# Kernel tuning notes

Measured on AMD Instinct MI355X. Metric: run time of the kernel, lower is better.

Reference implementation:

```python
import jax, jax.numpy as jnp
import numpy as np

EPS = 1e-6


def smooth(p):
    # smooth_distribution: clamp Bernoulli params away from {0,1}
    return jnp.clip(p, EPS, 1.0 - EPS)


def bern_logprob(p, x):
    # Bernoulli(p).log_prob(x) = x*log(p) + (1-x)*log(1-p)
    return x * jnp.log(p) + (1.0 - x) * jnp.log1p(-p)


def binary_row_reduce(A, b, k):
    # GF(2) Gaussian elimination on [A | b]; A:(k,n) binary float, b:(k,)
    M = jnp.concatenate([A, b[:, None]], axis=1)  # (k, n+1)
    rows = jnp.arange(k)
    for i in range(k):  # k is a small static int (25)
        col = M[:, i]
        cand = jnp.where((rows >= i) & (col > 0.5), rows, k)
        p = jnp.minimum(jnp.min(cand), k - 1)  # pivot row (fallback k-1 if none; prob ~0 for random A)
        ri, rp = M[i], M[p]
        M = M.at[i].set(rp)
        M = M.at[p].set(ri)
        elim = (M[:, i] > 0.5) & (rows != i)
        M = jnp.where(elim[:, None], jnp.mod(M + M[i], 2.0), M)
    return M[:, :-1], M[:, -1]


def compute_term1(logq, logp):
    # stable [sum_s q*log p]/[sum_s q], summed over batch; logq,logp: (S,B)
    m = jnp.max(logq, axis=0)                                  # (B,)
    w = jnp.exp(logq - m)                                      # (S,B)
    neg_num = m + jnp.log(jnp.sum(w * (-logp), axis=0))
    pos_den = m + jnp.log(jnp.sum(w, axis=0))
    return -jnp.sum(jnp.exp(neg_num - pos_den))


def setup_inputs() -> dict:
    key = jax.random.key(0)
    ks = jax.random.split(key, 5)
    nx, nz, B = 2048, 256, 512
    wr = float(np.sqrt(6.0 / (nx + nz)))
    xr = float(np.sqrt(6.0 / nx))
    zr = float(np.sqrt(6.0 / nz))
    U = jax.random.uniform(ks[0], (nz, nx), minval=-wr, maxval=wr)
    V = jax.random.uniform(ks[1], (nx, nz), minval=-wr, maxval=wr)
    x_bias = jax.random.uniform(ks[2], (nx,), minval=-xr, maxval=xr)
    z_bias = jax.random.uniform(ks[3], (nz,), minval=-zr, maxval=zr)
    xin = (jax.random.uniform(ks[4], (B, nx)) < 0.5).astype(jnp.float32)
    return {"xin": xin, "U": U, "V": V, "x_bias": x_bias, "z_bias": z_bias,
            "S": 10, "k": 25, "T": 30}


def reference(xin, U, V, x_bias, z_bias, S, k, T):
    dt = xin.dtype
    key = jax.random.key(42)
    kz, kx, kA, kb = jax.random.split(key, 4)

    # q(z|x) and samples  -------------------------------------------------
    q = smooth(jax.nn.sigmoid(xin @ U.T + z_bias))                     # (B, nz)
    samples_z = (jax.random.uniform(kz, (S,) + q.shape) < q).astype(dt)  # (S,B,nz)
    ps = smooth(jax.nn.sigmoid(jnp.einsum('sbz,xz->sbx', samples_z, V) + x_bias))  # (S,B,nx)
    xouts = (jax.random.uniform(kx, ps.shape) < ps).astype(dt)

    # projected ELBO over T random GF(2) hash constraints ------------------
    nz = U.shape[0]
    A_all = (jax.random.uniform(kA, (T, k, nz)) < 0.5).astype(dt)
    b_all = (jax.random.uniform(kb, (T, k)) < 0.5).astype(dt)
    pz = smooth(jax.nn.sigmoid(z_bias))                                # (nz,)

    def elbo_t(carry, Ab):
        A, b = Ab
        C, bp = binary_row_reduce(A, b, k)                             # (k,nz),(k,)
        proj = jnp.mod(jnp.einsum('sbz,kz->sbk', samples_z[:, :, k:], C[:, k:]) + bp, 2.0)
        sz = samples_z.at[:, :, :k].set(proj)                          # (S,B,nz)
        logq_zi = bern_logprob(q, sz).sum(axis=2)                      # (S,B)
        logp_z = bern_logprob(pz, sz).sum(axis=2)                      # (S,B)
        ps_t = smooth(jax.nn.sigmoid(jnp.einsum('sbz,xz->sbx', sz, V) + x_bias))
        logp_x = bern_logprob(ps_t, xin).sum(axis=2)                   # (S,B)
        logp = logp_z + logp_x
        term2 = compute_term1(logq_zi, logq_zi)
        term1 = compute_term1(logq_zi, logp)
        return carry, term1 - term2

    _, pelbos = jax.lax.scan(elbo_t, 0.0, (A_all, b_all))
    loss = -jnp.mean(pelbos)
    return q, samples_z, ps, xouts, loss
```

## Files before the change

### kernel.cpp

```cpp
#include <hip/hip_runtime.h>
#include <cstdint>

#define NX 2048
#define NZ 256
#define NB 512
#define NS 10
#define NK 25
#define NT 30
#define SBTOT (NS * NB)

#define LOG2E 1.4426950408889634f
#define LN2 0.6931471805599453f

#define OFF_Q 0
#define OFF_SAMP (NB * NZ)
#define OFF_PS (OFF_SAMP + SBTOT * NZ)
#define OFF_XO (OFF_PS + SBTOT * NX)
#define OFF_LOSS (OFF_XO + SBTOT * NX)

typedef unsigned long long ull;
typedef __bf16 bf16x8 __attribute__((ext_vector_type(8)));
typedef float f32x4 __attribute__((ext_vector_type(4)));
typedef uint32_t u32x2 __attribute__((ext_vector_type(2)));

__host__ __device__ inline void tf2x32(uint32_t k0, uint32_t k1, uint32_t x0, uint32_t x1,
                                       uint32_t& o0, uint32_t& o1) {
  uint32_t k2 = k0 ^ k1 ^ 0x1BD11BDAu;
  x0 += k0; x1 += k1;
#define TF_R(r) { x0 += x1; x1 = (x1 << (r)) | (x1 >> (32 - (r))); x1 ^= x0; }
  TF_R(13) TF_R(15) TF_R(26) TF_R(6)
  x0 += k1; x1 += k2 + 1u;
  TF_R(17) TF_R(29) TF_R(16) TF_R(24)
  x0 += k2; x1 += k0 + 2u;
  TF_R(13) TF_R(15) TF_R(26) TF_R(6)
  x0 += k0; x1 += k1 + 3u;
  TF_R(17) TF_R(29) TF_R(16) TF_R(24)
  x0 += k1; x1 += k2 + 4u;
  TF_R(13) TF_R(15) TF_R(26) TF_R(6)
  x0 += k2; x1 += k0 + 5u;
#undef TF_R
  o0 = x0; o1 = x1;
}

__device__ inline uint32_t tf_select(uint32_t k0, uint32_t k1, uint32_t i, uint32_t h) {
  bool lo = i < h;
  uint32_t x0 = lo ? i : i - h;
  uint32_t x1 = lo ? i + h : i;
  uint32_t o0, o1;
  tf2x32(k0, k1, x0, x1, o0, o1);
  return lo ? o0 : o1;
}

__device__ inline float tf_uniform(uint32_t k0, uint32_t k1, uint32_t i, uint32_t h) {
  uint32_t r = tf_select(k0, k1, i, h);
  return __uint_as_float(0x3f800000u | (r >> 9)) - 1.0f;
}

__device__ inline float sigclip(float a) {
  float p = 1.0f / (1.0f + __expf(-a));
  return fminf(fmaxf(p, 1e-6f), 1.0f - 1e-6f);
}

__device__ inline ushort f2bf(float f) {
  uint32_t u = __float_as_uint(f);
  return (ushort)((u + 0x7FFFu + ((u >> 16) & 1u)) >> 16);
}

__device__ inline float blockReduceSum256(float v, volatile float* s4) {
#pragma unroll
  for (int o = 32; o > 0; o >>= 1) v += __shfl_down(v, o);
  __syncthreads();
  if ((threadIdx.x & 63) == 0) s4[threadIdx.x >> 6] = v;
  __syncthreads();
  return s4[0] + s4[1] + s4[2] + s4[3];
}

__global__ __launch_bounds__(256) void kP0_prep(const float* __restrict__ V,
                                                const float* __restrict__ U,
                                                const float* __restrict__ xin,
                                                const float* __restrict__ z_bias,
                                                ushort* __restrict__ Vbf,
                                                ushort* __restrict__ Vkpad2,
                                                ushort* __restrict__ Uhi,
                                                ushort* __restrict__ Ulo,
                                                ushort* __restrict__ xinbf,
                                                float* __restrict__ baseq,
                                                float* __restrict__ d_lpz,
                                                float* __restrict__ basepz,
                                                double* __restrict__ loss_acc,
                                                uint32_t* __restrict__ done_ctr) {
  __shared__ float red[4];
  int tid = threadIdx.x;
  int e = blockIdx.x * 256 + tid;
  {
    int x = e >> 8, k = e & 255;
    float v = V[e];
    Vbf[e] = f2bf(v);
    if (k < 32) Vkpad2[x * 32 + k] = (k < NK) ? f2bf(v * LOG2E) : (ushort)0;
  }
  {
    float u = U[e];
    ushort hi = f2bf(u);
    Uhi[e] = hi;
    float hv = __uint_as_float((uint32_t)hi << 16);
    Ulo[e] = f2bf(u - hv);
  }
  {
    xinbf[e] = (xin[e] > 0.5f) ? (ushort)0x3F80 : (ushort)0;
    int e2 = e + NX * NZ;
    xinbf[e2] = (xin[e2] > 0.5f) ? (ushort)0x3F80 : (ushort)0;
  }
  if (e < NB) baseq[e] = 0.0f;
  if (blockIdx.x == 0) {
    if (tid == 0) { *loss_acc = 0.0; *done_ctr = 0u; }
    int z = tid;
    float pz = sigclip(z_bias[z]);
    float lp = __logf(pz), l1 = __logf(1.0f - pz);
    d_lpz[z] = lp - l1;
    float s = blockReduceSum256(l1, red);
    if (z == 0) *basepz = s;
  }
}

__global__ __launch_bounds__(256) void k1w_mfma(const ushort* __restrict__ xinbf,
                                                const ushort* __restrict__ Uhi,
                                                const ushort* __restrict__ Ulo,
                                                const float* __restrict__ z_bias,
                                                const float* __restrict__ xin,
                                                const ushort* __restrict__ Vkpad2,
                                                float* __restrict__ outq,
                                                float* __restrict__ d_lq,
                                                float* __restrict__ baseq,
                                                float* __restrict__ W,
                                                ull* __restrict__ Ct,
                                                uint32_t* __restrict__ bpmask,
                                                uint32_t kA0, uint32_t kA1,
                                                uint32_t kb0, uint32_t kb1) {
  __shared__ float red[4][16][17];
  __shared__ float wred[4][NK];
  __shared__ uint32_t Aw[NK][8];
  __shared__ uint32_t bbsh[NK];
  int tid = threadIdx.x;
  if (blockIdx.x >= 1024) {
    int t = blockIdx.x - 1024;
    if (tid < NK * 8) {
      int r = tid >> 3, c = tid & 7;
      const uint32_t hA = (uint32_t)NT * NK * NZ / 2;
      uint32_t base_i = (uint32_t)(t * NK + r) * NZ + c * 32;
      uint32_t w = 0;
      for (int zz = 0; zz < 32; ++zz) {
        uint32_t rr = tf_select(kA0, kA1, base_i + zz, hA);
        w |= ((rr >> 31) ^ 1u) << zz;
      }
      Aw[r][c] = w;
    }
    if (tid < NK) {
      const uint32_t hb = (uint32_t)NT * NK / 2;
      uint32_t rb = tf_select(kb0, kb1, (uint32_t)(t * NK + tid), hb);
      bbsh[tid] = (rb >> 31) ^ 1u;
    }
    __syncthreads();
    if (tid >= 64) return;
    int lane = tid;
    ull w0 = 0, w1 = 0, w2 = 0, w3 = 0;
    uint32_t bbit = 0;
    if (lane < NK) {
      w0 = (ull)Aw[lane][0] | ((ull)Aw[lane][1] << 32);
      w1 = (ull)Aw[lane][2] | ((ull)Aw[lane][3] << 32);
      w2 = (ull)Aw[lane][4] | ((ull)Aw[lane][5] << 32);
      w3 = (ull)Aw[lane][6] | ((ull)Aw[lane][7] << 32);
      bbit = bbsh[lane];
    }
    for (int i = 0; i < NK; ++i) {
      int mybit = (int)((w0 >> i) & 1ull);
      ull mask = __ballot(lane < NK && mybit);
      ull cand = mask & (~0ull << i);
      int p = cand ? __builtin_ctzll(cand) : (NK - 1);
      int srcl = (lane == i) ? p : ((lane == p) ? i : lane);
      w0 = __shfl(w0, srcl); w1 = __shfl(w1, srcl); w2 = __shfl(w2, srcl); w3 = __shfl(w3, srcl);
      bbit = __shfl(bbit, srcl);
      ull p0 = __shfl(w0, i), p1 = __shfl(w1, i), p2 = __shfl(w2, i), p3 = __shfl(w3, i);
      uint32_t pvb = __shfl(bbit, i);
      int nb2 = (int)((w0 >> i) & 1ull);
      if (lane < NK && lane != i && nb2) {
        w0 ^= p0; w1 ^= p1; w2 ^= p2; w3 ^= p3; bbit ^= pvb;
      }
    }
    if (lane < NK) {
      w0 &= ~((1ull << NK) - 1ull);
      ull* dstp = Ct + (size_t)(t * NK + lane) * 4;
      dstp[0] = w0; dstp[1] = w1; dstp[2] = w2; dstp[3] = w3;
    }
    ull bm = __ballot(lane < NK && bbit);
    if (lane == 0) bpmask[t] = (uint32_t)bm & 0x1FFFFFFu;
    return;
  }
  if (blockIdx.x < 512) {
    int wave = tid >> 6, lane = tid & 63, grp = lane >> 4, col = lane & 15;
    int b0 = (blockIdx.x >> 4) * 16;
    int z0 = (blockIdx.x & 15) * 16;
    f32x4 acc = {0.f, 0.f, 0.f, 0.f};
    const ushort* arow = xinbf + (size_t)(b0 + col) * NX + wave * 512 + grp * 8;
    const ushort* bhr = Uhi + (size_t)(z0 + col) * NX + wave * 512 + grp * 8;
    const ushort* blr = Ulo + (size_t)(z0 + col) * NX + wave * 512 + grp * 8;
#pragma unroll 4
    for (int s = 0; s < 16; ++s) {
      bf16x8 a = *(const bf16x8*)(arow + s * 32);
      bf16x8 bh = *(const bf16x8*)(bhr + s * 32);
      bf16x8 bl = *(const bf16x8*)(blr + s * 32);
      acc = __builtin_amdgcn_mfma_f32_16x16x32_bf16(a, bh, acc, 0, 0, 0);
      acc = __builtin_amdgcn_mfma_f32_16x16x32_bf16(a, bl, acc, 0, 0, 0);
    }
#pragma unroll
    for (int r = 0; r < 4; ++r) red[wave][grp * 4 + r][col] = acc[r];
    __syncthreads();
    int bi = tid >> 4, zi = tid & 15;
    float aa = red[0][bi][zi] + red[1][bi][zi] + red[2][bi][zi] + red[3][bi][zi] + z_bias[z0 + zi];
    int b = b0 + bi, z = z0 + zi;
    float q = sigclip(aa);
    outq[b * NZ + z] = q;
    float lq = __logf(q), l1 = __logf(1.0f - q);
    d_lq[b * NZ + z] = lq - l1;
    float s1 = l1;
#pragma unroll
    for (int o = 1; o < 16; o <<= 1) s1 += __shfl_xor(s1, o);
    if (zi == 0) atomicAdd(&baseq[b], s1);
    return;
  }
  int b = blockIdx.x - 512;
  float acc[NK];
#pragma unroll
  for (int j = 0; j < NK; ++j) acc[j] = 0.0f;
#pragma unroll
  for (int i = 0; i < 8; ++i) {
    int x = i * 256 + tid;
    float s = 1.0f - 2.0f * xin[(size_t)b * NX + x];
    const uint4* vp = (const uint4*)(Vkpad2 + (size_t)x * 32);
    uint4 q0 = vp[0], q1 = vp[1], q2 = vp[2], q3 = vp[3];
    uint32_t w[16] = {q0.x, q0.y, q0.z, q0.w, q1.x, q1.y, q1.z, q1.w,
                      q2.x, q2.y, q2.z, q2.w, q3.x, q3.y, q3.z, q3.w};
#pragma unroll
    for (int j = 0; j < NK; ++j) {
      uint32_t wd = w[j >> 1];
      float v = __uint_as_float((j & 1) ? (wd & 0xFFFF0000u) : (wd << 16));
      acc[j] = fmaf(s, v, acc[j]);
    }
  }
#pragma unroll
  for (int j = 0; j < NK; ++j) {
#pragma unroll
    for (int o = 1; o < 64; o <<= 1) acc[j] += __shfl_xor(acc[j], o);
  }
  if ((tid & 63) == 0) {
#pragma unroll
    for (int j = 0; j < NK; ++j) wred[tid >> 6][j] = acc[j];
  }
  __syncthreads();
  if (tid < NK) W[b * 32 + tid] = wred[0][tid] + wred[1][tid] + wred[2][tid] + wred[3][tid];
}

__global__ __launch_bounds__(256) void k2_samples(const float* __restrict__ q,
                                                  const float* __restrict__ d_lq,
                                                  const float* __restrict__ d_lpz,
                                                  const ull* __restrict__ Ct,
                                                  const uint32_t* __restrict__ bpmask,
                                                  const float* __restrict__ W,
                                                  float* __restrict__ samp_out,
                                                  ushort* __restrict__ samp16,
                                                  ull* __restrict__ Spack,
                                                  float* __restrict__ qtail,
                                                  float* __restrict__ ptail,
                                                  uint32_t* __restrict__ projb,
                                                  float* __restrict__ Syd,
                                                  uint32_t kz0, uint32_t kz1) {
  __shared__ float red[4];
  __shared__ ull sp_sh[4];
  int sb = blockIdx.x;
  int z = threadIdx.x;
  int b = sb & (NB - 1);
  uint32_t i = (uint32_t)sb * NZ + z;
  const uint32_t h = (uint32_t)SBTOT * NZ / 2;
  float u = tf_uniform(kz0, kz1, i, h);
  float qv = q[b * NZ + z];
  int smp = (u < qv) ? 1 : 0;
  __builtin_nontemporal_store((float)smp, samp_out + i);
  samp16[i] = smp ? (ushort)0x3F80 : (ushort)0;
  ull m = __ballot(smp);
  if ((z & 63) == 0) { Spack[sb * 4 + (z >> 6)] = m; sp_sh[z >> 6] = m; }
  float dq = (z >= NK && smp) ? d_lq[b * NZ + z] : 0.0f;
  float dp = (z >= NK && smp) ? d_lpz[z] : 0.0f;
  float sq = blockReduceSum256(dq, red);
  float sp = blockReduceSum256(dp, red);
  if (z == 0) { qtail[sb] = sq; ptail[sb] = sp; }
  if (z < 32) {
    int t = z;
    ull s0 = sp_sh[0], s1 = sp_sh[1], s2 = sp_sh[2], s3 = sp_sh[3];
    uint32_t s25 = (uint32_t)(s0 & 0x1FFFFFFull);
    const float* Wb = W + (size_t)b * 32;
    uint32_t out;
    float syd = 0.0f;
    if (t < NT) {
      uint32_t bp = bpmask[t];
      uint32_t pb = 0;
#pragma unroll
      for (int j = 0; j < NK; ++j) {
        const ull* C = Ct + (size_t)(t * NK + j) * 4;
        int par = __popcll(s0 & C[0]) + __popcll(s1 & C[1]) + __popcll(s2 & C[2]) + __popcll(s3 & C[3]);
        uint32_t bit = ((uint32_t)(par ^ (int)(bp >> j))) & 1u;
        pb |= bit << j;
        int d = (int)bit - (int)((s25 >> j) & 1u);
        syd = fmaf((float)d, Wb[j], syd);
      }
      out = pb;
    } else {
      out = s25;
    }
    projb[sb * 32 + t] = out;
    Syd[sb * 32 + t] = syd;
  }
}

__global__ __launch_bounds__(256) void k3m_gemm(const ushort* __restrict__ samp16,
                                                const ushort* __restrict__ Vbf,
                                                const float* __restrict__ x_bias,
                                                ushort* __restrict__ base2,
                                                float* __restrict__ ps_out,
                                                float* __restrict__ xo_out,
                                                uint32_t kx0, uint32_t kx1) {
  __shared__ __align__(16) char smem[2 * 2112 * 4];
  ushort* As = (ushort*)smem;
  ushort* Bs = (ushort*)(smem + 8192);
  float* Tt = (float*)smem;

  int tid = threadIdx.x;
  int wave = tid >> 6, lane = tid & 63, grp = lane >> 4, col = lane & 15;
  int x0 = blockIdx.x * 128;
  int sb0 = blockIdx.y * 32;
  f32x4 acc[2][4];
#pragma unroll
  for (int mi = 0; mi < 2; ++mi)
#pragma unroll
    for (int ni = 0; ni < 4; ++ni) acc[mi][ni] = (f32x4){0.f, 0.f, 0.f, 0.f};

  for (int k0 = 0; k0 < NZ; k0 += 32) {
    {
      int rowb = tid >> 2, kcb = (tid & 3) << 3;
      int sbrow = (rowb < 32) ? (sb0 + rowb) : (sb0 + 2528 + rowb);
      *(uint4*)&Bs[rowb * 32 + kcb] = *(const uint4*)&samp16[(size_t)sbrow * NZ + k0 + kcb];
#pragma unroll
      for (int c = tid; c < 512; c += 256) {
        int rowa = c >> 2, kca = (c & 3) << 3;
        *(uint4*)&As[rowa * 32 + kca] = *(const uint4*)&Vbf[(size_t)(x0 + rowa) * NZ + k0 + kca];
      }
    }
    __syncthreads();
    bf16x8 af[2], bfv[4];
#pragma unroll
    for (int mi = 0; mi < 2; ++mi)
      af[mi] = *(const bf16x8*)&As[(wave * 32 + mi * 16 + col) * 32 + grp * 8];
#pragma unroll
    for (int ni = 0; ni < 4; ++ni)
      bfv[ni] = *(const bf16x8*)&Bs[(ni * 16 + col) * 32 + grp * 8];
#pragma unroll
    for (int mi = 0; mi < 2; ++mi)
#pragma unroll
      for (int ni = 0; ni < 4; ++ni)
        acc[mi][ni] = __builtin_amdgcn_mfma_f32_16x16x32_bf16(af[mi], bfv[ni], acc[mi][ni], 0, 0, 0);
    __syncthreads();
  }

  const uint32_t HH = (uint32_t)(SBTOT / 2) * (uint32_t)NX;
#pragma unroll
  for (int pi = 0; pi < 2; ++pi) {
    __syncthreads();
#pragma unroll
    for (int mi = 0; mi < 2; ++mi) {
      int cbase = wave * 32 + mi * 16 + grp * 4;
      *(float4*)&Tt[col * 132 + cbase] = *(float4*)&acc[mi][pi];
      *(float4*)&Tt[2112 + col * 132 + cbase] = *(float4*)&acc[mi][pi + 2];
    }
    __syncthreads();
#pragma unroll
    for (int pass = 0; pass < 2; ++pass) {
      int r = pass * 8 + (tid >> 5);
      int c = (tid & 31) * 4;
      float4 t0 = *(float4*)&Tt[r * 132 + c];
      float4 t1 = *(float4*)&Tt[2112 + r * 132 + c];
      float4 xb4 = *(const float4*)(x_bias + x0 + c);
      int sb_a = sb0 + pi * 16 + r;
      size_t off_a = (size_t)sb_a * NX + x0 + c;
      size_t off_b = off_a + (size_t)HH;
      float a0 = t0.x + xb4.x, a1 = t0.y + xb4.y, a2 = t0.z + xb4.z, a3 = t0.w + xb4.w;
      float b0 = t1.x + xb4.x, b1 = t1.y + xb4.y, b2 = t1.z + xb4.z, b3 = t1.w + xb4.w;
      u32x2 bpa, bpb;
      bpa[0] = (uint32_t)f2bf(a0 * LOG2E) | ((uint32_t)f2bf(a1 * LOG2E) << 16);
      bpa[1] = (uint32_t)f2bf(a2 * LOG2E) | ((uint32_t)f2bf(a3 * LOG2E) << 16);
      bpb[0] = (uint32_t)f2bf(b0 * LOG2E) | ((uint32_t)f2bf(b1 * LOG2E) << 16);
      bpb[1] = (uint32_t)f2bf(b2 * LOG2E) | ((uint32_t)f2bf(b3 * LOG2E) << 16);
      *(u32x2*)(base2 + off_a) = bpa;
      *(u32x2*)(base2 + off_b) = bpb;
      f32x4 pva = {sigclip(a0), sigclip(a1), sigclip(a2), sigclip(a3)};
      f32x4 pvb = {sigclip(b0), sigclip(b1), sigclip(b2), sigclip(b3)};
      __builtin_nontemporal_store(pva, (f32x4*)(ps_out + off_a));
      __builtin_nontemporal_store(pvb, (f32x4*)(ps_out + off_b));
      uint32_t fi = (uint32_t)off_a;
      uint32_t r0, r1;
      f32x4 xva, xvb;
      tf2x32(kx0, kx1, fi + 0u, fi + 0u + HH, r0, r1);
      xva[0] = ((__uint_as_float(0x3f800000u | (r0 >> 9)) - 1.0f) < pva[0]) ? 1.0f : 0.0f;
      xvb[0] = ((__uint_as_float(0x3f800000u | (r1 >> 9)) - 1.0f) < pvb[0]) ? 1.0f : 0.0f;
      tf2x32(kx0, kx1, fi + 1u, fi + 1u + HH, r0, r1);
      xva[1] = ((__uint_as_float(0x3f800000u | (r0 >> 9)) - 1.0f) < pva[1]) ? 1.0f : 0.0f;
      xvb[1] = ((__uint_as_float(0x3f800000u | (r1 >> 9)) - 1.0f) < pvb[1]) ? 1.0f : 0.0f;
      tf2x32(kx0, kx1, fi + 2u, fi + 2u + HH, r0, r1);
      xva[2] = ((__uint_as_float(0x3f800000u | (r0 >> 9)) - 1.0f) < pva[2]) ? 1.0f : 0.0f;
      xvb[2] = ((__uint_as_float(0x3f800000u | (r1 >> 9)) - 1.0f) < pvb[2]) ? 1.0f : 0.0f;
      tf2x32(kx0, kx1, fi + 3u, fi + 3u + HH, r0, r1);
      xva[3] = ((__uint_as_float(0x3f800000u | (r0 >> 9)) - 1.0f) < pva[3]) ? 1.0f : 0.0f;
      xvb[3] = ((__uint_as_float(0x3f800000u | (r1 >> 9)) - 1.0f) < pvb[3]) ? 1.0f : 0.0f;
      __builtin_nontemporal_store(xva, (f32x4*)(xo_out + off_a));
      __builtin_nontemporal_store(xvb, (f32x4*)(xo_out + off_b));
    }
  }
}

__global__ __launch_bounds__(256) void k6_mfma(const ushort* __restrict__ base2,
                                               const ushort* __restrict__ Vkpad2,
                                               const float* __restrict__ xin,
                                               const uint32_t* __restrict__ projb,
                                               const ull* __restrict__ Spack,
                                               const float* __restrict__ Syd,
                                               float* __restrict__ logpx) {
  __shared__ float bvsm[NX];
  __shared__ float lsum[4][32];
  __shared__ float red[4];
  int sb = blockIdx.x;
  int b = sb & (NB - 1);
  int tid = threadIdx.x;
  int wave = tid >> 6, lane = tid & 63;
  int grp = lane >> 4, col = lane & 15;
  const uint4* b16p = (const uint4*)(base2 + (size_t)sb * NX);
  const float4* x4p = (const float4*)(xin + (size_t)b * NX);
  float sbacc = 0.0f;
  {
    uint4 bu = b16p[tid];
    float4 xv0 = x4p[tid * 2], xv1 = x4p[tid * 2 + 1];
    uint32_t wds[4] = {bu.x, bu.y, bu.z, bu.w};
    float bv[8];
#pragma unroll
    for (int j = 0; j < 8; ++j) {
      uint32_t wd = wds[j >> 1];
      bv[j] = __uint_as_float((j & 1) ? (wd & 0xFFFF0000u) : (wd << 16));
    }
    float sg[8] = {1.0f - 2.0f * xv0.x, 1.0f - 2.0f * xv0.y, 1.0f - 2.0f * xv0.z,
                   1.0f - 2.0f * xv0.w, 1.0f - 2.0f * xv1.x, 1.0f - 2.0f * xv1.y,
                   1.0f - 2.0f * xv1.z, 1.0f - 2.0f * xv1.w};
#pragma unroll
    for (int j = 0; j < 8; ++j) {
      bvsm[tid * 8 + j] = bv[j];
      sbacc = fmaf(sg[j], bv[j], sbacc);
    }
  }
  float Sb = blockReduceSum256(sbacc, red);
  uint32_t s25 = (uint32_t)(Spack[sb * 4] & 0x1FFFFFFull);
  uint32_t pb0 = projb[sb * 32 + col];
  uint32_t pb1 = projb[sb * 32 + 16 + col];
  bf16x8 a0, a1;
  union { ushort u; __bf16 hh; } cvt;
#pragma unroll
  for (int j = 0; j < 8; ++j) {
    int k = grp * 8 + j;
    int sbit = (int)((s25 >> k) & 1u);
    int d0 = (int)((pb0 >> k) & 1u) - sbit;
    int d1 = (int)((pb1 >> k) & 1u) - sbit;
    cvt.u = (ushort)(d0 == 0 ? 0 : (d0 > 0 ? 0x3F80 : 0xBF80)); a0[j] = cvt.hh;
    cvt.u = (ushort)(d1 == 0 ? 0 : (d1 > 0 ? 0x3F80 : 0xBF80)); a1[j] = cvt.hh;
  }
  float acca[8], pp[8];
#pragma unroll
  for (int r = 0; r < 8; ++r) { acca[r] = 0.0f; pp[r] = 1.0f; }
  const ushort* vkbase = Vkpad2 + (size_t)(wave * 512 + col) * 32 + grp * 8;
  const float* bvp = bvsm + wave * 512 + col;
#pragma unroll 4
  for (int i = 0; i < 32; ++i) {
    float bs = bvp[i * 16];
    bf16x8 bfr = *(const bf16x8*)(vkbase + (size_t)i * 16 * 32);
    f32x4 cb = {bs, bs, bs, bs};
    f32x4 c0 = __builtin_amdgcn_mfma_f32_16x16x32_bf16(a0, bfr, cb, 0, 0, 0);
    f32x4 c1 = __builtin_amdgcn_mfma_f32_16x16x32_bf16(a1, bfr, cb, 0, 0, 0);
#pragma unroll
    for (int r = 0; r < 4; ++r) {
      float y0 = c0[r];
      acca[r] += fabsf(y0);
      pp[r] = fmaf(pp[r], __builtin_amdgcn_exp2f(-fabsf(y0)), pp[r]);
      float y1 = c1[r];
      acca[4 + r] += fabsf(y1);
      pp[4 + r] = fmaf(pp[4 + r], __builtin_amdgcn_exp2f(-fabsf(y1)), pp[4 + r]);
    }
  }
#pragma unroll
  for (int r = 0; r < 8; ++r) {
    float m = 0.5f * acca[r] + __log2f(pp[r]);
#pragma unroll
    for (int off = 1; off < 16; off <<= 1) m += __shfl_xor(m, off);
    if (col == 0) {
      int t = (r < 4) ? (grp * 4 + r) : (16 + grp * 4 + (r - 4));
      lsum[wave][t] = m;
    }
  }
  __syncthreads();
  if (tid < NT) {
    float tot = lsum[0][tid] + lsum[1][tid] + lsum[2][tid] + lsum[3][tid];
    tot += 0.5f * (Sb + Syd[sb * 32 + tid]);
    logpx[(size_t)tid * SBTOT + sb] = -LN2 * tot;
  }
}

__global__ __launch_bounds__(64) void k7_reduce(const float* __restrict__ logpx,
                                                const uint32_t* __restrict__ projb,
                                                const float* __restrict__ qtail,
                                                const float* __restrict__ ptail,
                                                const float* __restrict__ baseq,
                                                const float* __restrict__ d_lq,
                                                const float* __restrict__ d_lpz,
                                                const float* __restrict__ basepz,
                                                double* __restrict__ loss_acc,
                                                uint32_t* __restrict__ done_ctr,
                                                float* __restrict__ out_loss) {
  int t = blockIdx.x;
  int chunk = blockIdx.y;
  int lane = threadIdx.x;
  int b = chunk * 64 + lane;
  float dlq[NK];
#pragma unroll
  for (int j = 0; j < NK; ++j) dlq[j] = d_lq[b * NZ + j];
  float bq = baseq[b];
  float bpz = *basepz;
  float lq[NS], lp[NS];
#pragma unroll
  for (int s = 0; s < NS; ++s) {
    int sb = s * NB + b;
    uint32_t m = projb[sb * 32 + t];
    float sq = 0.0f, spv = 0.0f;
#pragma unroll
    for (int j = 0; j < NK; ++j) {
      float on = (float)((m >> j) & 1u);
      sq += on * dlq[j];
      spv += on * d_lpz[j];
    }
    lq[s] = bq + qtail[sb] + sq;
    lp[s] = logpx[t * SBTOT + sb] + bpz + ptail[sb] + spv;
  }
  float mx = lq[0];
#pragma unroll
  for (int s = 1; s < NS; ++s) mx = fmaxf(mx, lq[s]);
  float den = 0.0f, num = 0.0f;
#pragma unroll
  for (int s = 0; s < NS; ++s) {
    float w = __expf(lq[s] - mx);
    den += w;
    num += w * (lq[s] - lp[s]);
  }
  double v = (double)(num / den);
#pragma unroll
  for (int o = 32; o > 0; o >>= 1) v += __shfl_down(v, o);
  if (lane == 0) {
    atomicAdd(loss_acc, v);
    __threadfence();
    uint32_t old = atomicAdd(done_ctr, 1u);
    if (old == (uint32_t)(NT * 8 - 1)) {
      double tot = atomicAdd(loss_acc, 0.0);
      *out_loss = (float)(tot / (double)NT);
    }
  }
}

extern "C" void kernel_launch(void* const* d_in, const int* in_sizes, int n_in,
                              void* d_out, int out_size, void* d_ws, size_t ws_size,
                              hipStream_t stream) {
  const float* xin = (const float*)d_in[0];
  const float* U = (const float*)d_in[1];
  const float* V = (const float*)d_in[2];
  const float* x_bias = (const float*)d_in[3];
  const float* z_bias = (const float*)d_in[4];
  float* out = (float*)d_out;

  char* p = (char*)d_ws;
  ushort* base2 = (ushort*)p;             p += (size_t)SBTOT * NX * 2;
  float* d_lq = (float*)p;                p += (size_t)NB * NZ * 4;
  float* baseq = (float*)p;               p += (size_t)NB * 4;
  float* d_lpz = (float*)p;               p += (size_t)NZ * 4;
  float* basepz = (float*)p;              p += 16;
  ull* Spack = (ull*)p;                   p += (size_t)SBTOT * 4 * 8;
  float* qtail = (float*)p;               p += (size_t)SBTOT * 4;
  float* ptail = (float*)p;               p += (size_t)SBTOT * 4;
  ull* Ct = (ull*)p;                      p += (size_t)NT * NK * 4 * 8;
  uint32_t* bpm = (uint32_t*)p;           p += 128;
  uint32_t* projb = (uint32_t*)p;         p += (size_t)SBTOT * 32 * 4;
  float* Syd = (float*)p;                 p += (size_t)SBTOT * 32 * 4;
  float* logpx = (float*)p;               p += (size_t)NT * SBTOT * 4;
  double* loss_acc = (double*)p;          p += 64;
  uint32_t* done_ctr = (uint32_t*)p;      p += 64;
  ushort* Vkpad2 = (ushort*)p;            p += (size_t)NX * 32 * 2;
  ushort* Vbf = (ushort*)p;               p += (size_t)NX * NZ * 2;
  ushort* samp16 = (ushort*)p;            p += (size_t)SBTOT * NZ * 2;
  float* W = (float*)p;                   p += (size_t)NB * 32 * 4;
  ushort* Uhi = (ushort*)p;               p += (size_t)NZ * NX * 2;
  ushort* Ulo = (ushort*)p;               p += (size_t)NZ * NX * 2;
  ushort* xinbf = (ushort*)p;             p += (size_t)NB * NX * 2;
  (void)ws_size; (void)in_sizes; (void)n_in; (void)out_size;

  uint32_t o0[4], o1[4];
  for (int j = 0; j < 4; ++j) tf2x32(0u, 42u, (uint32_t)j, (uint32_t)(4 + j), o0[j], o1[j]);
  uint32_t kz0 = o0[0], kz1 = o0[1];
  uint32_t kx0 = o0[2], kx1 = o0[3];
  uint32_t kA0 = o1[0], kA1 = o1[1];
  uint32_t kb0 = o1[2], kb1 = o1[3];

  kP0_prep<<<NX * NZ / 256, 256, 0, stream>>>(V, U, xin, z_bias, Vbf, Vkpad2,
                                              Uhi, Ulo, xinbf, baseq, d_lpz, basepz,
                                              loss_acc, done_ctr);
  k1w_mfma<<<1024 + NT, 256, 0, stream>>>(xinbf, Uhi, Ulo, z_bias, xin, Vkpad2,
                                          out + OFF_Q, d_lq, baseq, W,
                                          Ct, bpm, kA0, kA1, kb0, kb1);
  k2_samples<<<SBTOT, 256, 0, stream>>>(out + OFF_Q, d_lq, d_lpz, Ct, bpm, W,
                                        out + OFF_SAMP, samp16, Spack, qtail, ptail,
                                        projb, Syd, kz0, kz1);
  dim3 g3(NX / 128, SBTOT / 64);
  k3m_gemm<<<g3, 256, 0, stream>>>(samp16, Vbf, x_bias, base2,
                                   out + OFF_PS, out + OFF_XO, kx0, kx1);
  k6_mfma<<<SBTOT, 256, 0, stream>>>(base2, Vkpad2, xin, projb, Spack, Syd, logpx);
  dim3 g7(NT, 8);
  k7_reduce<<<g7, 64, 0, stream>>>(logpx, projb, qtail, ptail, baseq, d_lq,
                                   d_lpz, basepz, loss_acc, done_ctr, out + OFF_LOSS);
}
```

Measured before the change: 254.6 us.

## Split GEMM and logpx kernels into staged launches that overlap their work

The k3m GEMM is split into two parts: the first 40 row-tiles run on their own, and the remaining 40 row-tiles are co-scheduled in one mixed launch with k6 logpx blocks whose base2 inputs are already complete. A final k6 launch covers the remaining samples. The goal is to fill the GPU tail and overlap the compute-bound GEMM with the exp-heavy k6 work instead of serialising them. Separately, k6 now starts the MFMAs from zero and adds the bias afterwards instead of passing it as the accumulator, which may change register pressure. In exchange the change adds an extra launch and a divergent mixed kernel whose shared-memory size may limit k6 occupancy.

```diff
diff --git a/kernel.cpp b/kernel.cpp
--- a/kernel.cpp
+++ b/kernel.cpp
@@ -320,22 +320,20 @@
   }
 }
 
-__global__ __launch_bounds__(256) void k3m_gemm(const ushort* __restrict__ samp16,
-                                                const ushort* __restrict__ Vbf,
-                                                const float* __restrict__ x_bias,
-                                                ushort* __restrict__ base2,
-                                                float* __restrict__ ps_out,
-                                                float* __restrict__ xo_out,
-                                                uint32_t kx0, uint32_t kx1) {
-  __shared__ __align__(16) char smem[2 * 2112 * 4];
+__device__ inline void k3m_body(int x0, int sb0, char* smem,
+                                const ushort* __restrict__ samp16,
+                                const ushort* __restrict__ Vbf,
+                                const float* __restrict__ x_bias,
+                                ushort* __restrict__ base2,
+                                float* __restrict__ ps_out,
+                                float* __restrict__ xo_out,
+                                uint32_t kx0, uint32_t kx1) {
   ushort* As = (ushort*)smem;
   ushort* Bs = (ushort*)(smem + 8192);
   float* Tt = (float*)smem;
 
   int tid = threadIdx.x;
   int wave = tid >> 6, lane = tid & 63, grp = lane >> 4, col = lane & 15;
-  int x0 = blockIdx.x * 128;
-  int sb0 = blockIdx.y * 32;
   f32x4 acc[2][4];
 #pragma unroll
   for (int mi = 0; mi < 2; ++mi)
@@ -424,17 +422,17 @@
   }
 }
 
-__global__ __launch_bounds__(256) void k6_mfma(const ushort* __restrict__ base2,
-                                               const ushort* __restrict__ Vkpad2,
-                                               const float* __restrict__ xin,
-                                               const uint32_t* __restrict__ projb,
-                                               const ull* __restrict__ Spack,
-                                               const float* __restrict__ Syd,
-                                               float* __restrict__ logpx) {
-  __shared__ float bvsm[NX];
-  __shared__ float lsum[4][32];
-  __shared__ float red[4];
-  int sb = blockIdx.x;
+__device__ inline void k6_body(int sb, char* smem,
+                               const ushort* __restrict__ base2,
+                               const ushort* __restrict__ Vkpad2,
+                               const float* __restrict__ xin,
+                               const uint32_t* __restrict__ projb,
+                               const ull* __restrict__ Spack,
+                               const float* __restrict__ Syd,
+                               float* __restrict__ logpx) {
+  float* bvsm = (float*)smem;
+  float (*lsum)[32] = (float(*)[32])(smem + 8192);
+  float* red = (float*)(smem + 8704);
   int b = sb & (NB - 1);
   int tid = threadIdx.x;
   int wave = tid >> 6, lane = tid & 63;
@@ -480,20 +478,20 @@
 #pragma unroll
   for (int r = 0; r < 8; ++r) { acca[r] = 0.0f; pp[r] = 1.0f; }
   const ushort* vkbase = Vkpad2 + (size_t)(wave * 512 + col) * 32 + grp * 8;
-  const float* bvp = bvsm + wave * 512 + col;
 #pragma unroll 4
   for (int i = 0; i < 32; ++i) {
-    float bs = bvp[i * 16];
+    int x = (wave * 32 + i) * 16 + col;
     bf16x8 bfr = *(const bf16x8*)(vkbase + (size_t)i * 16 * 32);
-    f32x4 cb = {bs, bs, bs, bs};
-    f32x4 c0 = __builtin_amdgcn_mfma_f32_16x16x32_bf16(a0, bfr, cb, 0, 0, 0);
-    f32x4 c1 = __builtin_amdgcn_mfma_f32_16x16x32_bf16(a1, bfr, cb, 0, 0, 0);
+    f32x4 c0 = {0.f, 0.f, 0.f, 0.f}, c1 = {0.f, 0.f, 0.f, 0.f};
+    c0 = __builtin_amdgcn_mfma_f32_16x16x32_bf16(a0, bfr, c0, 0, 0, 0);
+    c1 = __builtin_amdgcn_mfma_f32_16x16x32_bf16(a1, bfr, c1, 0, 0, 0);
+    float bs = bvsm[x];
 #pragma unroll
     for (int r = 0; r < 4; ++r) {
-      float y0 = c0[r];
+      float y0 = bs + c0[r];
       acca[r] += fabsf(y0);
       pp[r] = fmaf(pp[r], __builtin_amdgcn_exp2f(-fabsf(y0)), pp[r]);
-      float y1 = c1[r];
+      float y1 = bs + c1[r];
       acca[4 + r] += fabsf(y1);
       pp[4 + r] = fmaf(pp[4 + r], __builtin_amdgcn_exp2f(-fabsf(y1)), pp[4 + r]);
     }
@@ -514,6 +512,57 @@
     tot += 0.5f * (Sb + Syd[sb * 32 + tid]);
     logpx[(size_t)tid * SBTOT + sb] = -LN2 * tot;
   }
+}
+
+__global__ __launch_bounds__(256) void k3m_gemm(const ushort* __restrict__ samp16,
+                                                const ushort* __restrict__ Vbf,
+                                                const float* __restrict__ x_bias,
+                                                ushort* __restrict__ base2,
+                                                float* __restrict__ ps_out,
+                                                float* __restrict__ xo_out,
+                                                uint32_t kx0, uint32_t kx1,
+                                                int ybase) {
+  __shared__ __align__(16) char smem[2 * 2112 * 4];
+  k3m_body(blockIdx.x * 128, (ybase + blockIdx.y) * 32, smem,
+           samp16, Vbf, x_bias, base2, ps_out, xo_out, kx0, kx1);
+}
+
+__global__ __launch_bounds__(256) void k36_mix(const ushort* __restrict__ samp16,
+                                               const ushort* __restrict__ Vbf,
+                                               const float* __restrict__ x_bias,
+                                               ushort* __restrict__ base2,
+                                               float* __restrict__ ps_out,
+                                               float* __restrict__ xo_out,
+                                               uint32_t kx0, uint32_t kx1,
+                                               const ushort* __restrict__ Vkpad2,
+                                               const float* __restrict__ xin,
+                                               const uint32_t* __restrict__ projb,
+                                               const ull* __restrict__ Spack,
+                                               const float* __restrict__ Syd,
+                                               float* __restrict__ logpx) {
+  __shared__ __align__(16) char smem[2 * 2112 * 4];
+  int bx = blockIdx.x;
+  if (bx < 640) {
+    k3m_body((bx & 15) * 128, (40 + (bx >> 4)) * 32, smem,
+             samp16, Vbf, x_bias, base2, ps_out, xo_out, kx0, kx1);
+  } else {
+    int i = bx - 640;
+    int sb = (i < 1280) ? i : i + 1280;
+    k6_body(sb, smem, base2, Vkpad2, xin, projb, Spack, Syd, logpx);
+  }
+}
+
+__global__ __launch_bounds__(256) void k6_solo(const ushort* __restrict__ base2,
+                                               const ushort* __restrict__ Vkpad2,
+                                               const float* __restrict__ xin,
+                                               const uint32_t* __restrict__ projb,
+                                               const ull* __restrict__ Spack,
+                                               const float* __restrict__ Syd,
+                                               float* __restrict__ logpx) {
+  __shared__ __align__(16) char smem[8720];
+  int i = blockIdx.x;
+  int sb = (i < 1280) ? (1280 + i) : (2560 + i);
+  k6_body(sb, smem, base2, Vkpad2, xin, projb, Spack, Syd, logpx);
 }
 
 __global__ __launch_bounds__(64) void k7_reduce(const float* __restrict__ logpx,
@@ -626,11 +675,15 @@
   k2_samples<<<SBTOT, 256, 0, stream>>>(out + OFF_Q, d_lq, d_lpz, Ct, bpm, W,
                                         out + OFF_SAMP, samp16, Spack, qtail, ptail,
                                         projb, Syd, kz0, kz1);
-  dim3 g3(NX / 128, SBTOT / 64);
-  k3m_gemm<<<g3, 256, 0, stream>>>(samp16, Vbf, x_bias, base2,
-                                   out + OFF_PS, out + OFF_XO, kx0, kx1);
-  k6_mfma<<<SBTOT, 256, 0, stream>>>(base2, Vkpad2, xin, projb, Spack, Syd, logpx);
+  dim3 g3a(NX / 128, 40);
+  k3m_gemm<<<g3a, 256, 0, stream>>>(samp16, Vbf, x_bias, base2,
+                                    out + OFF_PS, out + OFF_XO, kx0, kx1, 0);
+  k36_mix<<<640 + 2560, 256, 0, stream>>>(samp16, Vbf, x_bias, base2,
+                                          out + OFF_PS, out + OFF_XO, kx0, kx1,
+                                          Vkpad2, xin, projb, Spack, Syd, logpx);
+  k6_solo<<<2560, 256, 0, stream>>>(base2, Vkpad2, xin, projb, Spack, Syd, logpx);
   dim3 g7(NT, 8);
   k7_reduce<<<g7, 64, 0, stream>>>(logpx, projb, qtail, ptail, baseq, d_lq,
-                                   d_lpz, basepz, loss_acc, done_ctr, out + OFF_LOSS);
-}
+                                   d_lpz, basepz, loss_acc, done_ctr,
+                                   out + OFF_LOSS);
+}
```

Result: slower. 281.9 us (+10.7%).

## Fuse decoder GEMM with per-constraint logpx MFMA kernel via shared-memory tile

Applied to the files above, without the earlier changes.

Merges the decoder GEMM kernel and the per-constraint log p(x) kernel into one. The bf16 logits stay in shared memory for the block's 64 sample rows and 128 x-columns instead of going through a global base2 buffer. Each block computes partial logpx sums for its x-slice and accumulates them with atomicAdd into logpx, which k2 now zero-initialises. This removes the global write and re-read of the logits and one launch. In exchange it adds 16 atomics per row per constraint, doubles shared memory per block, and makes the float summation order nondeterministic.

```diff
diff --git a/kernel.cpp b/kernel.cpp
--- a/kernel.cpp
+++ b/kernel.cpp
@@ -272,6 +272,7 @@
                                                   float* __restrict__ ptail,
                                                   uint32_t* __restrict__ projb,
                                                   float* __restrict__ Syd,
+                                                  float* __restrict__ logpx,
                                                   uint32_t kz0, uint32_t kz1) {
   __shared__ float red[4];
   __shared__ ull sp_sh[4];
@@ -312,6 +313,7 @@
         syd = fmaf((float)d, Wb[j], syd);
       }
       out = pb;
+      logpx[(size_t)t * SBTOT + sb] = 0.0f;
     } else {
       out = s25;
     }
@@ -320,17 +322,23 @@
   }
 }
 
-__global__ __launch_bounds__(256) void k3m_gemm(const ushort* __restrict__ samp16,
-                                                const ushort* __restrict__ Vbf,
-                                                const float* __restrict__ x_bias,
-                                                ushort* __restrict__ base2,
-                                                float* __restrict__ ps_out,
-                                                float* __restrict__ xo_out,
-                                                uint32_t kx0, uint32_t kx1) {
-  __shared__ __align__(16) char smem[2 * 2112 * 4];
+__global__ __launch_bounds__(256) void k36_fused(const ushort* __restrict__ samp16,
+                                                 const ushort* __restrict__ Vbf,
+                                                 const float* __restrict__ x_bias,
+                                                 const ushort* __restrict__ Vkpad2,
+                                                 const float* __restrict__ xin,
+                                                 const uint32_t* __restrict__ projb,
+                                                 const ull* __restrict__ Spack,
+                                                 const float* __restrict__ Syd,
+                                                 float* __restrict__ ps_out,
+                                                 float* __restrict__ xo_out,
+                                                 float* __restrict__ logpx,
+                                                 uint32_t kx0, uint32_t kx1) {
+  __shared__ __align__(16) char smem[16896 + 16896];
   ushort* As = (ushort*)smem;
   ushort* Bs = (ushort*)(smem + 8192);
   float* Tt = (float*)smem;
+  ushort* bs16 = (ushort*)(smem + 16896);
 
   int tid = threadIdx.x;
   int wave = tid >> 6, lane = tid & 63, grp = lane >> 4, col = lane & 15;
@@ -387,7 +395,8 @@
       float4 t0 = *(float4*)&Tt[r * 132 + c];
       float4 t1 = *(float4*)&Tt[2112 + r * 132 + c];
       float4 xb4 = *(const float4*)(x_bias + x0 + c);
-      int sb_a = sb0 + pi * 16 + r;
+      int rowa = pi * 16 + r;
+      int sb_a = sb0 + rowa;
       size_t off_a = (size_t)sb_a * NX + x0 + c;
       size_t off_b = off_a + (size_t)HH;
       float a0 = t0.x + xb4.x, a1 = t0.y + xb4.y, a2 = t0.z + xb4.z, a3 = t0.w + xb4.w;
@@ -397,8 +406,8 @@
       bpa[1] = (uint32_t)f2bf(a2 * LOG2E) | ((uint32_t)f2bf(a3 * LOG2E) << 16);
       bpb[0] = (uint32_t)f2bf(b0 * LOG2E) | ((uint32_t)f2bf(b1 * LOG2E) << 16);
       bpb[1] = (uint32_t)f2bf(b2 * LOG2E) | ((uint32_t)f2bf(b3 * LOG2E) << 16);
-      *(u32x2*)(base2 + off_a) = bpa;
-      *(u32x2*)(base2 + off_b) = bpb;
+      *(u32x2*)&bs16[rowa * 132 + c] = bpa;
+      *(u32x2*)&bs16[(32 + rowa) * 132 + c] = bpb;
       f32x4 pva = {sigclip(a0), sigclip(a1), sigclip(a2), sigclip(a3)};
       f32x4 pvb = {sigclip(b0), sigclip(b1), sigclip(b2), sigclip(b3)};
       __builtin_nontemporal_store(pva, (f32x4*)(ps_out + off_a));
@@ -422,97 +431,68 @@
       __builtin_nontemporal_store(xvb, (f32x4*)(xo_out + off_b));
     }
   }
-}
-
-__global__ __launch_bounds__(256) void k6_mfma(const ushort* __restrict__ base2,
-                                               const ushort* __restrict__ Vkpad2,
-                                               const float* __restrict__ xin,
-                                               const uint32_t* __restrict__ projb,
-                                               const ull* __restrict__ Spack,
-                                               const float* __restrict__ Syd,
-                                               float* __restrict__ logpx) {
-  __shared__ float bvsm[NX];
-  __shared__ float lsum[4][32];
-  __shared__ float red[4];
-  int sb = blockIdx.x;
-  int b = sb & (NB - 1);
-  int tid = threadIdx.x;
-  int wave = tid >> 6, lane = tid & 63;
-  int grp = lane >> 4, col = lane & 15;
-  const uint4* b16p = (const uint4*)(base2 + (size_t)sb * NX);
-  const float4* x4p = (const float4*)(xin + (size_t)b * NX);
-  float sbacc = 0.0f;
-  {
-    uint4 bu = b16p[tid];
-    float4 xv0 = x4p[tid * 2], xv1 = x4p[tid * 2 + 1];
-    uint32_t wds[4] = {bu.x, bu.y, bu.z, bu.w};
-    float bv[8];
+  __syncthreads();
+
+  for (int s = 0; s < 16; ++s) {
+    int rowl = wave * 16 + s;
+    int sb = (rowl < 32) ? (sb0 + rowl) : (sb0 + 2528 + rowl);
+    int b = sb & (NB - 1);
+    uint32_t s25 = (uint32_t)(Spack[sb * 4] & 0x1FFFFFFull);
+    uint32_t pb0 = projb[sb * 32 + col];
+    uint32_t pb1 = projb[sb * 32 + 16 + col];
+    bf16x8 a0, a1;
+    union { ushort u; __bf16 hh; } cvt;
 #pragma unroll
     for (int j = 0; j < 8; ++j) {
-      uint32_t wd = wds[j >> 1];
-      bv[j] = __uint_as_float((j & 1) ? (wd & 0xFFFF0000u) : (wd << 16));
-    }
-    float sg[8] = {1.0f - 2.0f * xv0.x, 1.0f - 2.0f * xv0.y, 1.0f - 2.0f * xv0.z,
-                   1.0f - 2.0f * xv0.w, 1.0f - 2.0f * xv1.x, 1.0f - 2.0f * xv1.y,
-                   1.0f - 2.0f * xv1.z, 1.0f - 2.0f * xv1.w};
-#pragma unroll
-    for (int j = 0; j < 8; ++j) {
-      bvsm[tid * 8 + j] = bv[j];
-      sbacc = fmaf(sg[j], bv[j], sbacc);
-    }
-  }
-  float Sb = blockReduceSum256(sbacc, red);
-  uint32_t s25 = (uint32_t)(Spack[sb * 4] & 0x1FFFFFFull);
-  uint32_t pb0 = projb[sb * 32 + col];
-  uint32_t pb1 = projb[sb * 32 + 16 + col];
-  bf16x8 a0, a1;
-  union { ushort u; __bf16 hh; } cvt;
-#pragma unroll
-  for (int j = 0; j < 8; ++j) {
-    int k = grp * 8 + j;
-    int sbit = (int)((s25 >> k) & 1u);
-    int d0 = (int)((pb0 >> k) & 1u) - sbit;
-    int d1 = (int)((pb1 >> k) & 1u) - sbit;
-    cvt.u = (ushort)(d0 == 0 ? 0 : (d0 > 0 ? 0x3F80 : 0xBF80)); a0[j] = cvt.hh;
-    cvt.u = (ushort)(d1 == 0 ? 0 : (d1 > 0 ? 0x3F80 : 0xBF80)); a1[j] = cvt.hh;
-  }
-  float acca[8], pp[8];
-#pragma unroll
-  for (int r = 0; r < 8; ++r) { acca[r] = 0.0f; pp[r] = 1.0f; }
-  const ushort* vkbase = Vkpad2 + (size_t)(wave * 512 + col) * 32 + grp * 8;
-  const float* bvp = bvsm + wave * 512 + col;
-#pragma unroll 4
-  for (int i = 0; i < 32; ++i) {
-    float bs = bvp[i * 16];
-    bf16x8 bfr = *(const bf16x8*)(vkbase + (size_t)i * 16 * 32);
-    f32x4 cb = {bs, bs, bs, bs};
-    f32x4 c0 = __builtin_amdgcn_mfma_f32_16x16x32_bf16(a0, bfr, cb, 0, 0, 0);
-    f32x4 c1 = __builtin_amdgcn_mfma_f32_16x16x32_bf16(a1, bfr, cb, 0, 0, 0);
-#pragma unroll
-    for (int r = 0; r < 4; ++r) {
-      float y0 = c0[r];
-      acca[r] += fabsf(y0);
-      pp[r] = fmaf(pp[r], __builtin_amdgcn_exp2f(-fabsf(y0)), pp[r]);
-      float y1 = c1[r];
-      acca[4 + r] += fabsf(y1);
-      pp[4 + r] = fmaf(pp[4 + r], __builtin_amdgcn_exp2f(-fabsf(y1)), pp[4 + r]);
-    }
-  }
-#pragma unroll
-  for (int r = 0; r < 8; ++r) {
-    float m = 0.5f * acca[r] + __log2f(pp[r]);
-#pragma unroll
-    for (int off = 1; off < 16; off <<= 1) m += __shfl_xor(m, off);
-    if (col == 0) {
-      int t = (r < 4) ? (grp * 4 + r) : (16 + grp * 4 + (r - 4));
-      lsum[wave][t] = m;
-    }
-  }
-  __syncthreads();
-  if (tid < NT) {
-    float tot = lsum[0][tid] + lsum[1][tid] + lsum[2][tid] + lsum[3][tid];
-    tot += 0.5f * (Sb + Syd[sb * 32 + tid]);
-    logpx[(size_t)tid * SBTOT + sb] = -LN2 * tot;
+      int k = grp * 8 + j;
+      int sbit = (int)((s25 >> k) & 1u);
+      int d0 = (int)((pb0 >> k) & 1u) - sbit;
+      int d1 = (int)((pb1 >> k) & 1u) - sbit;
+      cvt.u = (ushort)(d0 == 0 ? 0 : (d0 > 0 ? 0x3F80 : 0xBF80)); a0[j] = cvt.hh;
+      cvt.u = (ushort)(d1 == 0 ? 0 : (d1 > 0 ? 0x3F80 : 0xBF80)); a1[j] = cvt.hh;
+    }
+    float acca[8], pp[8];
+#pragma unroll
+    for (int r = 0; r < 8; ++r) { acca[r] = 0.0f; pp[r] = 1.0f; }
+    float sacc = 0.0f;
+    const float* xinrow = xin + (size_t)b * NX + x0;
+#pragma unroll 2
+    for (int i = 0; i < 8; ++i) {
+      int xl = i * 16 + col;
+      bf16x8 bfr = *(const bf16x8*)(Vkpad2 + (size_t)(x0 + xl) * 32 + grp * 8);
+      float bs = __uint_as_float((uint32_t)bs16[rowl * 132 + xl] << 16);
+      float sg = 1.0f - 2.0f * xinrow[xl];
+      sacc = fmaf(sg, bs, sacc);
+      f32x4 c0 = {0.f, 0.f, 0.f, 0.f}, c1 = {0.f, 0.f, 0.f, 0.f};
+      c0 = __builtin_amdgcn_mfma_f32_16x16x32_bf16(a0, bfr, c0, 0, 0, 0);
+      c1 = __builtin_amdgcn_mfma_f32_16x16x32_bf16(a1, bfr, c1, 0, 0, 0);
+#pragma unroll
+      for (int r = 0; r < 4; ++r) {
+        float y0 = bs + c0[r];
+        acca[r] += fabsf(y0);
+        pp[r] = fmaf(pp[r], __builtin_amdgcn_exp2f(-fabsf(y0)), pp[r]);
+        float y1 = bs + c1[r];
+        acca[4 + r] += fabsf(y1);
+        pp[4 + r] = fmaf(pp[4 + r], __builtin_amdgcn_exp2f(-fabsf(y1)), pp[4 + r]);
+      }
+    }
+    float sbt = sacc;
+#pragma unroll
+    for (int off = 1; off < 16; off <<= 1) sbt += __shfl_xor(sbt, off);
+#pragma unroll
+    for (int r = 0; r < 8; ++r) {
+      float m = 0.5f * acca[r] + __log2f(pp[r]);
+#pragma unroll
+      for (int off = 1; off < 16; off <<= 1) m += __shfl_xor(m, off);
+      if (col == 0) {
+        int t = (r < 4) ? (grp * 4 + r) : (16 + grp * 4 + (r - 4));
+        if (t < NT) {
+          float contrib = m + 0.5f * sbt;
+          if (x0 == 0) contrib += 0.5f * Syd[sb * 32 + t];
+          atomicAdd(&logpx[(size_t)t * SBTOT + sb], -LN2 * contrib);
+        }
+      }
+    }
   }
 }
 
@@ -608,7 +588,7 @@
   ushort* Uhi = (ushort*)p;               p += (size_t)NZ * NX * 2;
   ushort* Ulo = (ushort*)p;               p += (size_t)NZ * NX * 2;
   ushort* xinbf = (ushort*)p;             p += (size_t)NB * NX * 2;
-  (void)ws_size; (void)in_sizes; (void)n_in; (void)out_size;
+  (void)base2; (void)ws_size; (void)in_sizes; (void)n_in; (void)out_size;
 
   uint32_t o0[4], o1[4];
   for (int j = 0; j < 4; ++j) tf2x32(0u, 42u, (uint32_t)j, (uint32_t)(4 + j), o0[j], o1[j]);
@@ -625,12 +605,13 @@
                                           Ct, bpm, kA0, kA1, kb0, kb1);
   k2_samples<<<SBTOT, 256, 0, stream>>>(out + OFF_Q, d_lq, d_lpz, Ct, bpm, W,
                                         out + OFF_SAMP, samp16, Spack, qtail, ptail,
-                                        projb, Syd, kz0, kz1);
-  dim3 g3(NX / 128, SBTOT / 64);
-  k3m_gemm<<<g3, 256, 0, stream>>>(samp16, Vbf, x_bias, base2,
-                                   out + OFF_PS, out + OFF_XO, kx0, kx1);
-  k6_mfma<<<SBTOT, 256, 0, stream>>>(base2, Vkpad2, xin, projb, Spack, Syd, logpx);
+                                        projb, Syd, logpx, kz0, kz1);
+  dim3 g36(NX / 128, SBTOT / 64);
+  k36_fused<<<g36, 256, 0, stream>>>(samp16, Vbf, x_bias, Vkpad2, xin,
+                                     projb, Spack, Syd,
+                                     out + OFF_PS, out + OFF_XO, logpx, kx0, kx1);
   dim3 g7(NT, 8);
   k7_reduce<<<g7, 64, 0, stream>>>(logpx, projb, qtail, ptail, baseq, d_lq,
-                                   d_lpz, basepz, loss_acc, done_ctr, out + OFF_LOSS);
-}
+                                   d_lpz, basepz, loss_acc, done_ctr,
+                                   out + OFF_LOSS);
+}
```

After: 421.0 us. 65.3% more time.
